# Performance work log

Measured on AMD Instinct MI355X. Metric: run time of the kernel, lower is better.

## Reference

```python
import jax, jax.numpy as jnp
import numpy as np
from math import sqrt

B, N, CS, H, D, K = 8, 256, 512, 8, 64, 32
NB = 2 * K + 1          # no_bins = 65
CT = 2048               # c_transition
INF = 1e9
WL = sqrt(0.5)          # w_L
EPS = 1e-5


def setup_inputs() -> dict:
    key = jax.random.key(0)
    ks = jax.random.split(key, 10)
    sc = 0.02
    return {
        "s": jax.random.normal(ks[0], (B, N, CS), jnp.float32),
        "masks": jnp.ones((B, N), jnp.bool_),
        "wq": jax.random.normal(ks[1], (CS, D * H), jnp.float32) * sc,
        "wk": jax.random.normal(ks[2], (CS, D * H), jnp.float32) * sc,
        "wv": jax.random.normal(ks[3], (CS, D * H), jnp.float32) * sc,
        "wb": jax.random.normal(ks[4], (NB, H), jnp.float32) * sc,
        "wo": jax.random.normal(ks[5], ((NB + D) * H, CS), jnp.float32) * sc,
        "bo": jnp.zeros((CS,), jnp.float32),
        "ln1_g": jnp.ones((CS,), jnp.float32),
        "ln1_b": jnp.zeros((CS,), jnp.float32),
        "w1": jax.random.normal(ks[6], (CS, CT), jnp.float32) * sc,
        "b1": jnp.zeros((CT,), jnp.float32),
        "w2": jax.random.normal(ks[7], (CT, CS), jnp.float32) * sc,
        "b2": jnp.zeros((CS,), jnp.float32),
        "ln2_g": jnp.ones((CS,), jnp.float32),
        "ln2_b": jnp.zeros((CS,), jnp.float32),
    }


def _layernorm(x, g, b):
    m = jnp.mean(x, -1, keepdims=True)
    v = jnp.var(x, -1, keepdims=True)
    return (x - m) * jax.lax.rsqrt(v + EPS) * g + b


def _heads(x):  # [B,N,D*H] -> [B,H,N,D]  (torch: reshape(B,N,D,H) then move H forward)
    return jnp.transpose(x.reshape(B, N, D, H), (0, 3, 1, 2))


def reference(s, masks, wq, wk, wv, wb, wo, bo, ln1_g, ln1_b, w1, b1, w2, b2, ln2_g, ln2_b):
    mf = masks.astype(s.dtype)                       # [B,N]
    sq = mf[:, :, None] * mf[:, None, :]             # [B,N,N]

    # relative position one-hot, clipped to [-K, K] -> [N,N,NB]
    r = jnp.arange(N)
    dmat = jnp.clip(r[:, None] - r[None, :], -K, K) + K
    relpos_base = jax.nn.one_hot(dmat, NB, dtype=s.dtype)
    relpos = relpos_base[None] * sq[..., None]       # [B,N,N,NB]

    b_bias = jnp.einsum('bijc,ch->bhij', relpos, wb)  # [B,H,N,N]

    q = _heads(s @ wq)                               # [B,H,N,D]
    k = _heads(s @ wk)
    v = _heads(s @ wv)

    logits = WL * (jnp.einsum('bhid,bhjd->bhij', q, k) / sqrt(D) + b_bias)
    logits = logits - INF * (1.0 - sq)[:, None]      # mask
    a = jax.nn.softmax(logits, axis=-1)              # [B,H,N,N]

    # pairwise aggregation and value aggregation (einsum avoids [B,H,N,N,NB] blowup)
    o_pair = jnp.einsum('bhij,bijc->bhic', a, relpos)  # [B,H,N,NB]
    o = jnp.einsum('bhij,bhjd->bhid', a, v)            # [B,H,N,D]

    op = jnp.transpose(o_pair, (0, 2, 1, 3)).reshape(B, N, H * NB)
    ov = jnp.transpose(o, (0, 2, 1, 3)).reshape(B, N, H * D)
    embd = jnp.concatenate([op, ov], axis=-1) @ wo + bo   # [B,N,CS]

    x = _layernorm(s + embd, ln1_g, ln1_b)
    ff = jax.nn.relu(x @ w1 + b1) @ w2 + b2
    x = _layernorm(x + ff, ln2_g, ln2_b)
    return x, a
```

## Files before the change

kernel.cpp:

```cpp
#include <hip/hip_runtime.h>
#include <hip/hip_bf16.h>
#include <cstdint>

#define B_ 8
#define N_ 256
#define CS_ 512
#define H_ 8
#define D_ 64
#define K_ 32
#define NB_ 65
#define CT_ 2048
#define WL_ 0.70710678118654752f

typedef __attribute__((ext_vector_type(8))) short bf16x8;
typedef __attribute__((ext_vector_type(4))) float f32x4;

#define GLOBAL_AS __attribute__((address_space(1)))
#define LDS_AS __attribute__((address_space(3)))

__device__ __forceinline__ void async16(void* lds, const void* g) {
  __builtin_amdgcn_global_load_lds((const GLOBAL_AS uint32_t*)g,
                                   (LDS_AS uint32_t*)lds, 16, 0, 0);
}

__device__ __forceinline__ ushort f2bf(float v) {
  __hip_bfloat16 hb = __float2bfloat16(v);
  return *(ushort*)&hb;
}

__device__ __forceinline__ float bf2f(ushort u) {
  union { uint32_t ui; float f; } cv; cv.ui = (uint32_t)u << 16;
  return cv.f;
}

template<int TN>
__device__ __forceinline__ void stage_tile(
    const ushort* __restrict__ A, const ushort* __restrict__ Bt,
    ushort* As, ushort* Bs, int bm, int bn, int Kd, int k0, int srow, int sg) {
  const int RP = TN / 8;
#pragma unroll
  for (int r = 0; r < 64 / RP; ++r) {
    int row = r * RP + srow;
    int gl = sg ^ (row & 7);
    async16(&As[row * 64 + sg * 8], A + (size_t)(bm + row) * Kd + k0 + gl * 8);
  }
#pragma unroll
  for (int r = 0; r < 8; ++r) {
    int row = r * RP + srow;
    int gl = sg ^ (row & 7);
    async16(&Bs[row * 64 + sg * 8], Bt + (size_t)(bn + row) * Kd + k0 + gl * 8);
  }
}

template<int TN>
__global__ __launch_bounds__(TN, 2) void gemm_bf16(
    const ushort* __restrict__ A, const ushort* __restrict__ Bt,
    const float* __restrict__ bias, float* __restrict__ C,
    ushort* __restrict__ Cb, int M, int Nc, int Kd, int flags) {
  __shared__ ushort As[2][64 * 64];
  __shared__ ushort Bs[2][TN * 64];
  int tid = threadIdx.x;
  int bm = blockIdx.y * 64, bn = blockIdx.x * TN;
  int S = gridDim.z, z = blockIdx.z;
  int T = Kd >> 6;
  int it0 = (z * T) / S, it1 = ((z + 1) * T) / S;
  if (flags & 8)  C  += (size_t)z * M * Nc;
  if (flags & 32) Cb += (size_t)z * M * Nc;
  int w = tid >> 6, l = tid & 63;
  int lm = l & 15, lq = l >> 4;
  int srow = tid >> 3;
  int sg = tid & 7;

  f32x4 acc[4][4];
#pragma unroll
  for (int i = 0; i < 4; ++i)
#pragma unroll
    for (int j = 0; j < 4; ++j) acc[i][j] = (f32x4){0.f, 0.f, 0.f, 0.f};

  stage_tile<TN>(A, Bt, &As[0][0], &Bs[0][0], bm, bn, Kd, it0 << 6, srow, sg);

  for (int it = it0; it < it1; ++it) {
    int cur = (it - it0) & 1;
    __syncthreads();
    if (it + 1 < it1) {
      int nxt = cur ^ 1;
      stage_tile<TN>(A, Bt, &As[nxt][0], &Bs[nxt][0], bm, bn, Kd,
                     (it + 1) << 6, srow, sg);
    }
#pragma unroll
    for (int kk = 0; kk < 2; ++kk) {
      bf16x8 af[4], bfr[4];
#pragma unroll
      for (int i = 0; i < 4; ++i) {
        int ma = 16 * i + lm;
        af[i] = *(const bf16x8*)&As[cur][ma * 64 + ((kk * 4 + lq) ^ (ma & 7)) * 8];
        int nb = w * 64 + 16 * i + lm;
        bfr[i] = *(const bf16x8*)&Bs[cur][nb * 64 + ((kk * 4 + lq) ^ (nb & 7)) * 8];
      }
#pragma unroll
      for (int i = 0; i < 4; ++i)
#pragma unroll
        for (int j = 0; j < 4; ++j)
          acc[i][j] = __builtin_amdgcn_mfma_f32_16x16x32_bf16(
              af[i], bfr[j], acc[i][j], 0, 0, 0);
    }
  }
  __syncthreads();

  int bcol0 = bn + w * 64;
  int lr = l >> 3, lc = l & 7;
  ushort* Tb = &Bs[0][w * 4096];

  if (flags & 16) {
    int which = bcol0 >> 9;
    int hh = (bcol0 & 511) >> 6;
    int b = bm >> 8, nn0 = bm & 255;
    if (which == 2) {
#pragma unroll
      for (int j = 0; j < 4; ++j)
#pragma unroll
        for (int i = 0; i < 4; ++i) {
          ushort pk[4];
#pragma unroll
          for (int r = 0; r < 4; ++r) pk[r] = f2bf(acc[i][j][r]);
          *(uint2*)&Tb[(16 * j + lm) * 64 + 16 * i + lq * 4] = *(uint2*)pk;
        }
    } else {
#pragma unroll
      for (int j = 0; j < 4; ++j)
#pragma unroll
        for (int i = 0; i < 4; ++i)
#pragma unroll
          for (int r = 0; r < 4; ++r)
            Tb[(16 * i + lq * 4 + r) * 64 + 16 * j + lm] = f2bf(acc[i][j][r]);
    }
    __asm__ __volatile__("" ::: "memory");
    ushort* dstb = Cb + (size_t)which * 1048576 + (size_t)(b * 8 + hh) * 16384;
#pragma unroll
    for (int p = 0; p < 8; ++p) {
      int rowL = p * 8 + lr;
      bf16x8 vv = *(const bf16x8*)&Tb[rowL * 64 + lc * 8];
      if (which == 2)
        *(bf16x8*)(dstb + (size_t)rowL * 256 + nn0 + lc * 8) = vv;
      else
        *(bf16x8*)(dstb + (size_t)(nn0 + rowL) * 64 + lc * 8) = vv;
    }
    return;
  }
  if (flags & 4) {
#pragma unroll
    for (int j = 0; j < 4; ++j) {
      float bv = ((flags & 1) && z == 0) ? bias[bcol0 + 16 * j + lm] : 0.f;
#pragma unroll
      for (int i = 0; i < 4; ++i)
#pragma unroll
        for (int r = 0; r < 4; ++r) {
          float v = acc[i][j][r] + bv;
          if (flags & 2) v = fmaxf(v, 0.f);
          Tb[(16 * i + lq * 4 + r) * 64 + 16 * j + lm] = f2bf(v);
        }
    }
    __asm__ __volatile__("" ::: "memory");
#pragma unroll
    for (int p = 0; p < 8; ++p) {
      int rowL = p * 8 + lr;
      bf16x8 vv = *(const bf16x8*)&Tb[rowL * 64 + lc * 8];
      *(bf16x8*)(Cb + (size_t)(bm + rowL) * Nc + bcol0 + lc * 8) = vv;
    }
    return;
  }
#pragma unroll
  for (int j = 0; j < 4; ++j) {
    int col = bcol0 + 16 * j + lm;
    float bv = ((flags & 1) && z == 0) ? bias[col] : 0.f;
#pragma unroll
    for (int i = 0; i < 4; ++i)
#pragma unroll
      for (int r = 0; r < 4; ++r) {
        int row = bm + 16 * i + lq * 4 + r;
        float v = acc[i][j][r] + bv;
        if (flags & 2) v = fmaxf(v, 0.f);
        C[(size_t)row * Nc + col] = v;
      }
  }
}

__global__ __launch_bounds__(256) void prep_all(
    const float* __restrict__ s, __hip_bfloat16* __restrict__ s_bf,
    const float* __restrict__ wq, const float* __restrict__ wk,
    const float* __restrict__ wv, const float* __restrict__ wo,
    const float* __restrict__ w1, const float* __restrict__ w2,
    __hip_bfloat16* __restrict__ wqkvT, __hip_bfloat16* __restrict__ wopT,
    __hip_bfloat16* __restrict__ w1T, __hip_bfloat16* __restrict__ w2T) {
  int blk = blockIdx.x;
  if (blk < 512) {
    int i = blk * 256 + threadIdx.x;
    float4 a = ((const float4*)s)[i * 2];
    float4 c = ((const float4*)s)[i * 2 + 1];
    ushort pk[8] = {f2bf(a.x), f2bf(a.y), f2bf(a.z), f2bf(a.w),
                    f2bf(c.x), f2bf(c.y), f2bf(c.z), f2bf(c.w)};
    *(uint4*)&((ushort*)s_bf)[i * 8] = *(uint4*)pk;
    return;
  }
  blk -= 512;
  __shared__ float tile[32][33];
  const float* src;
  __hip_bfloat16* dst;
  int R, C, Kpad, tX, tIdx, whichBase = -1;
  if (blk < 768) {
    int zz = blk >> 8; tIdx = blk & 255;
    src = zz == 0 ? wq : zz == 1 ? wk : wv;
    dst = wqkvT; whichBase = zz * 512; R = 512; C = 512; Kpad = 512; tX = 16;
  } else if (blk < 1312) {
    tIdx = blk - 768; src = wo; dst = wopT; R = 1032; C = 512; Kpad = 1088; tX = 16;
  } else if (blk < 2336) {
    tIdx = blk - 1312; src = w1; dst = w1T; R = 512; C = 2048; Kpad = 512; tX = 64;
  } else {
    tIdx = blk - 2336; src = w2; dst = w2T; R = 2048; C = 512; Kpad = 2048; tX = 16;
  }
  int c0 = (tIdx % tX) * 32, r0 = (tIdx / tX) * 32;
  int tx = threadIdx.x & 7, ty = threadIdx.x >> 3;
  {
    int r = r0 + ty, c = c0 + tx * 4;
    float4 v = (r < R) ? *(const float4*)&src[(size_t)r * C + c]
                       : (float4){0.f, 0.f, 0.f, 0.f};
    tile[ty][tx * 4 + 0] = v.x;
    tile[ty][tx * 4 + 1] = v.y;
    tile[ty][tx * 4 + 2] = v.z;
    tile[ty][tx * 4 + 3] = v.w;
  }
  __syncthreads();
  {
    int cc = c0 + ty;
    int k = r0 + tx * 4;
    float a0 = tile[tx * 4 + 0][ty];
    float a1 = tile[tx * 4 + 1][ty];
    float a2 = tile[tx * 4 + 2][ty];
    float a3 = tile[tx * 4 + 3][ty];
    int n = (whichBase >= 0) ? (whichBase + (cc & 7) * 64 + (cc >> 3)) : cc;
    ushort pk[4] = {f2bf(a0), f2bf(a1), f2bf(a2), f2bf(a3)};
    *(uint2*)&dst[(size_t)n * Kpad + k] = *(uint2*)pk;
  }
}

__global__ __launch_bounds__(128) void attn_fused(
    const ushort* __restrict__ qh, const ushort* __restrict__ kh,
    const ushort* __restrict__ vT, const int* __restrict__ masks,
    const float* __restrict__ wb, float* __restrict__ a_out,
    ushort* __restrict__ cat) {
  int strip = blockIdx.x & 7, bh = blockIdx.x >> 3;
  int h = bh & 7, b = bh >> 3;
  __shared__ ushort Ks[256 * 64];
  __shared__ ushort Ps[32 * 64];
  __shared__ float wbs[NB_];
  __shared__ float mfj[256];
  int tid = threadIdx.x;
  int srow = tid >> 3, sg = tid & 7;
#pragma unroll
  for (int rr = 0; rr < 16; ++rr) {
    int row = rr * 16 + srow;
    int gl = sg ^ (row & 7);
    async16(&Ks[row * 64 + sg * 8],
            kh + ((size_t)bh * 256 + row) * 64 + gl * 8);
  }
  int w = tid >> 6, l = tid & 63, lm = l & 15, lq = l >> 4;
  bf16x8 qf[2];
  {
    const ushort* qrow =
        qh + ((size_t)bh * 256 + strip * 32 + w * 16 + lm) * 64 + lq * 8;
    qf[0] = *(const bf16x8*)qrow;
    qf[1] = *(const bf16x8*)(qrow + 32);
  }
  if (tid < NB_) wbs[tid] = wb[tid * H_ + h];
  mfj[tid]       = (masks[b * 256 + tid] != 0) ? 1.f : 0.f;
  mfj[tid + 128] = (masks[b * 256 + tid + 128] != 0) ? 1.f : 0.f;
  __syncthreads();

  f32x4 acc[16];
#pragma unroll
  for (int ct = 0; ct < 16; ++ct) {
    int krow = ct * 16 + lm;
    bf16x8 kf0 = *(const bf16x8*)&Ks[krow * 64 + ((lq) ^ (krow & 7)) * 8];
    bf16x8 kf1 = *(const bf16x8*)&Ks[krow * 64 + ((4 + lq) ^ (krow & 7)) * 8];
    f32x4 zf = (f32x4){0.f, 0.f, 0.f, 0.f};
    zf = __builtin_amdgcn_mfma_f32_16x16x32_bf16(qf[0], kf0, zf, 0, 0, 0);
    acc[ct] = __builtin_amdgcn_mfma_f32_16x16x32_bf16(qf[1], kf1, zf, 0, 0, 0);
  }
  int ibase = strip * 32 + w * 16 + lq * 4;
  float mfi[4];
#pragma unroll
  for (int r = 0; r < 4; ++r) mfi[r] = mfj[ibase + r];
#pragma unroll
  for (int ct = 0; ct < 16; ++ct) {
    int j = ct * 16 + lm;
    float mj = mfj[j];
#pragma unroll
    for (int r = 0; r < 4; ++r) {
      int i = ibase + r;
      int diff = i - j;
      int cb = diff < -K_ ? 0 : (diff > K_ ? 2 * K_ : diff + K_);
      float sq = mfi[r] * mj;
      acc[ct][r] = WL_ * (acc[ct][r] * 0.125f + wbs[cb] * sq) - 1e9f * (1.f - sq);
    }
  }
  float mx[4], sm[4];
#pragma unroll
  for (int r = 0; r < 4; ++r) {
    float m = acc[0][r];
#pragma unroll
    for (int ct = 1; ct < 16; ++ct) m = fmaxf(m, acc[ct][r]);
#pragma unroll
    for (int o = 1; o < 16; o <<= 1) m = fmaxf(m, __shfl_xor(m, o, 64));
    mx[r] = m;
  }
#pragma unroll
  for (int ct = 0; ct < 16; ++ct)
#pragma unroll
    for (int r = 0; r < 4; ++r) acc[ct][r] = __expf(acc[ct][r] - mx[r]);
#pragma unroll
  for (int r = 0; r < 4; ++r) {
    float s = 0.f;
#pragma unroll
    for (int ct = 0; ct < 16; ++ct) s += acc[ct][r];
#pragma unroll
    for (int o = 1; o < 16; o <<= 1) s += __shfl_xor(s, o, 64);
    sm[r] = 1.f / s;
  }
  float p0[4] = {0.f, 0.f, 0.f, 0.f}, p64[4] = {0.f, 0.f, 0.f, 0.f};
#pragma unroll
  for (int ct = 0; ct < 16; ++ct) {
    int j = ct * 16 + lm;
    float mj = mfj[j];
#pragma unroll
    for (int r = 0; r < 4; ++r) {
      int i = ibase + r;
      float aval = acc[ct][r] * sm[r];
      a_out[((size_t)bh * 256 + i) * 256 + j] = aval;
      float val = aval * mfi[r] * mj;
      int diff = i - j;
      if (diff <= -K_)      p0[r] += val;
      else if (diff >= K_)  p64[r] += val;
      else cat[((size_t)(b * 256 + i)) * 1088 + h * 65 + diff + K_] = f2bf(val);
    }
  }
#pragma unroll
  for (int r = 0; r < 4; ++r)
#pragma unroll
    for (int o = 1; o < 16; o <<= 1) {
      p0[r]  += __shfl_xor(p0[r], o, 64);
      p64[r] += __shfl_xor(p64[r], o, 64);
    }
  if (lm == 0) {
#pragma unroll
    for (int r = 0; r < 4; ++r) {
      int i = ibase + r;
      cat[((size_t)(b * 256 + i)) * 1088 + h * 65 + 0]      = f2bf(p0[r]);
      cat[((size_t)(b * 256 + i)) * 1088 + h * 65 + 2 * K_] = f2bf(p64[r]);
    }
  }
#pragma unroll
  for (int r = 0; r < 4; ++r) {
    int i = ibase + r;
#pragma unroll
    for (int t = 0; t < 4; ++t) {
      int c = 1 + lm + 16 * t;
      if (c < 64) {
        int j = i - c + K_;
        if (j < 0 || j > 255)
          cat[((size_t)(b * 256 + i)) * 1088 + h * 65 + c] = 0;
      }
    }
  }
  if (h == 0) {
    for (int idx = tid; idx < 32 * 56; idx += 128) {
      int r = idx / 56, c = 1032 + (idx - r * 56);
      cat[((size_t)(b * 256 + strip * 32 + r)) * 1088 + c] = 0;
    }
  }
  f32x4 acc2[4];
#pragma unroll
  for (int nt = 0; nt < 4; ++nt) acc2[nt] = (f32x4){0.f, 0.f, 0.f, 0.f};
  const ushort* vbase = vT + (size_t)bh * 16384;
#pragma unroll
  for (int qt = 0; qt < 4; ++qt) {
    bf16x8 vf0[4], vf1[4];
#pragma unroll
    for (int nt = 0; nt < 4; ++nt) {
      const ushort* vrow = vbase + (size_t)(nt * 16 + lm) * 256 + qt * 64 + lq * 8;
      vf0[nt] = *(const bf16x8*)vrow;
      vf1[nt] = *(const bf16x8*)(vrow + 32);
    }
#pragma unroll
    for (int ctl = 0; ctl < 4; ++ctl) {
      int ct = qt * 4 + ctl;
#pragma unroll
      for (int r = 0; r < 4; ++r) {
        int rowl = w * 16 + lq * 4 + r;
        int g = ctl * 2 + (lm >> 3);
        Ps[rowl * 64 + ((g ^ (rowl & 7)) << 3) + (lm & 7)] =
            f2bf(acc[ct][r] * sm[r]);
      }
    }
    int prow = w * 16 + lm;
#pragma unroll
    for (int kst = 0; kst < 2; ++kst) {
      bf16x8 af = *(const bf16x8*)&Ps[prow * 64 + (((kst * 4 + lq) ^ (prow & 7)) << 3)];
#pragma unroll
      for (int nt = 0; nt < 4; ++nt)
        acc2[nt] = __builtin_amdgcn_mfma_f32_16x16x32_bf16(
            af, kst ? vf1[nt] : vf0[nt], acc2[nt], 0, 0, 0);
    }
  }
#pragma unroll
  for (int nt = 0; nt < 4; ++nt) {
    int d = nt * 16 + lm;
#pragma unroll
    for (int r = 0; r < 4; ++r) {
      int i = ibase + r;
      cat[((size_t)(b * 256 + i)) * 1088 + 520 + h * 64 + d] = f2bf(acc2[nt][r]);
    }
  }
}

__global__ __launch_bounds__(128) void ln_sum(
    const float* __restrict__ x1, const ushort* __restrict__ xp,
    int S, int stride, const float* __restrict__ g,
    const float* __restrict__ bta, float* __restrict__ out,
    __hip_bfloat16* __restrict__ out_bf) {
  __shared__ float redA[2], redB[2];
  int row = blockIdx.x, tid = threadIdx.x;
  size_t base = (size_t)row * 512;
  float4 v = *(const float4*)(x1 + base + tid * 4);
  for (int s = 0; s < S; ++s) {
    uint2 p = *(const uint2*)(xp + (size_t)s * stride + base + tid * 4);
    v.x += bf2f((ushort)(p.x & 0xffff));
    v.y += bf2f((ushort)(p.x >> 16));
    v.z += bf2f((ushort)(p.y & 0xffff));
    v.w += bf2f((ushort)(p.y >> 16));
  }
  float su = v.x + v.y + v.z + v.w;
  float sq = v.x * v.x + v.y * v.y + v.z * v.z + v.w * v.w;
#pragma unroll
  for (int o = 32; o > 0; o >>= 1) {
    su += __shfl_xor(su, o, 64);
    sq += __shfl_xor(sq, o, 64);
  }
  int w = tid >> 6;
  if ((tid & 63) == 0) { redA[w] = su; redB[w] = sq; }
  __syncthreads();
  su = redA[0] + redA[1]; sq = redB[0] + redB[1];
  float mean = su * (1.f / 512.f);
  float var = sq * (1.f / 512.f) - mean * mean;
  float inv = rsqrtf(var + 1e-5f);
  float4 gv = *(const float4*)(g + tid * 4);
  float4 bv = *(const float4*)(bta + tid * 4);
  float4 o4;
  o4.x = (v.x - mean) * inv * gv.x + bv.x;
  o4.y = (v.y - mean) * inv * gv.y + bv.y;
  o4.z = (v.z - mean) * inv * gv.z + bv.z;
  o4.w = (v.w - mean) * inv * gv.w + bv.w;
  *(float4*)(out + base + tid * 4) = o4;
  if (out_bf) {
    ushort pk[4] = {f2bf(o4.x), f2bf(o4.y), f2bf(o4.z), f2bf(o4.w)};
    *(uint2*)&((ushort*)out_bf)[base + tid * 4] = *(uint2*)pk;
  }
}

extern "C" void kernel_launch(void* const* d_in, const int* in_sizes, int n_in,
                              void* d_out, int out_size, void* d_ws, size_t ws_size,
                              hipStream_t stream) {
  const float* s     = (const float*)d_in[0];
  const int*   masks = (const int*)d_in[1];
  const float* wq = (const float*)d_in[2];
  const float* wk = (const float*)d_in[3];
  const float* wv = (const float*)d_in[4];
  const float* wb = (const float*)d_in[5];
  const float* wo = (const float*)d_in[6];
  const float* bo = (const float*)d_in[7];
  const float* ln1_g = (const float*)d_in[8];
  const float* ln1_b = (const float*)d_in[9];
  const float* w1 = (const float*)d_in[10];
  const float* b1 = (const float*)d_in[11];
  const float* w2 = (const float*)d_in[12];
  const float* b2 = (const float*)d_in[13];
  const float* ln2_g = (const float*)d_in[14];
  const float* ln2_b = (const float*)d_in[15];

  float* out_x = (float*)d_out;
  float* out_a = out_x + 1048576;

  float* ws = (float*)d_ws;
  ushort* embd_part = (ushort*)(ws + 0);
  float* xbuf       = ws + 4194304;
  ushort* ff_part   = (ushort*)(ws + 5242880);
  ushort* qkv_bf    = (ushort*)(ws + 9437184);
  ushort* q_bf = qkv_bf;
  ushort* k_bf = qkv_bf + 1048576;
  ushort* v_bf = qkv_bf + 2097152;
  ushort* cat_bf = (ushort*)(ws + 10223616);
  __hip_bfloat16* h_bf  = (__hip_bfloat16*)(ws + 11337728);
  __hip_bfloat16* s_bf  = (__hip_bfloat16*)(ws + 13434880);
  __hip_bfloat16* x_bf  = (__hip_bfloat16*)(ws + 13959168);
  __hip_bfloat16* wqkvT = (__hip_bfloat16*)(ws + 14483456);
  __hip_bfloat16* wopT  = (__hip_bfloat16*)(ws + 14876672);
  __hip_bfloat16* w1T   = (__hip_bfloat16*)(ws + 15155200);
  __hip_bfloat16* w2T   = (__hip_bfloat16*)(ws + 15679488);

  dim3 blk(256);
  prep_all<<<dim3(3872), blk, 0, stream>>>(s, s_bf, wq, wk, wv, wo, w1, w2,
                                           wqkvT, wopT, w1T, w2T);
  gemm_bf16<128><<<dim3(12, 32, 1), dim3(128), 0, stream>>>(
      (const ushort*)s_bf, (const ushort*)wqkvT, nullptr, nullptr,
      qkv_bf, 2048, 1536, 512, 16);
  attn_fused<<<dim3(512), dim3(128), 0, stream>>>(q_bf, k_bf, v_bf, masks, wb,
                                                  out_a, cat_bf);
  gemm_bf16<256><<<dim3(2, 32, 8), blk, 0, stream>>>(
      cat_bf, (const ushort*)wopT, bo, nullptr, embd_part,
      2048, 512, 1088, 1 | 4 | 32);
  ln_sum<<<dim3(2048), dim3(128), 0, stream>>>(s, embd_part, 8, 1048576,
                                               ln1_g, ln1_b, xbuf, x_bf);
  gemm_bf16<256><<<dim3(8, 32, 1), blk, 0, stream>>>(
      (const ushort*)x_bf, (const ushort*)w1T, b1, nullptr, (ushort*)h_bf,
      2048, 2048, 512, 1 | 2 | 4);
  gemm_bf16<256><<<dim3(2, 32, 8), blk, 0, stream>>>(
      (const ushort*)h_bf, (const ushort*)w2T, b2, nullptr, ff_part,
      2048, 512, 2048, 1 | 4 | 32);
  ln_sum<<<dim3(2048), dim3(128), 0, stream>>>(xbuf, ff_part, 8, 1048576,
                                               ln2_g, ln2_b, out_x, nullptr);
}
```

Measured before the change: 177.1 us.

## Triple-buffer GEMM LDS pipeline with prefetch depth two, unify tile to 64x128

Replaces the double-buffered GEMM K-loop with a three-stage LDS ring that prefetches two tiles ahead, using an explicit vmcnt wait and a raw barrier instead of __syncthreads. The GEMM template is collapsed to a single 128-thread, 64x128 tile shape. The output and FFN2 split-K GEMMs go from split 8 to split 4, with correspondingly more N blocks, and the layernorm reduction sums 4 partials instead of 8. This aims to hide global-load latency better and cut partial-sum traffic, at the cost of more LDS per block and redundant clamped prefetches at the end of the loop.

```diff
diff --git a/kernel.cpp b/kernel.cpp
--- a/kernel.cpp
+++ b/kernel.cpp
@@ -33,34 +33,31 @@
   return cv.f;
 }
 
-template<int TN>
 __device__ __forceinline__ void stage_tile(
     const ushort* __restrict__ A, const ushort* __restrict__ Bt,
     ushort* As, ushort* Bs, int bm, int bn, int Kd, int k0, int srow, int sg) {
-  const int RP = TN / 8;
-#pragma unroll
-  for (int r = 0; r < 64 / RP; ++r) {
-    int row = r * RP + srow;
+#pragma unroll
+  for (int r = 0; r < 4; ++r) {
+    int row = r * 16 + srow;
     int gl = sg ^ (row & 7);
     async16(&As[row * 64 + sg * 8], A + (size_t)(bm + row) * Kd + k0 + gl * 8);
   }
 #pragma unroll
   for (int r = 0; r < 8; ++r) {
-    int row = r * RP + srow;
+    int row = r * 16 + srow;
     int gl = sg ^ (row & 7);
     async16(&Bs[row * 64 + sg * 8], Bt + (size_t)(bn + row) * Kd + k0 + gl * 8);
   }
 }
 
-template<int TN>
-__global__ __launch_bounds__(TN, 2) void gemm_bf16(
+__global__ __launch_bounds__(128) void gemm_bf16(
     const ushort* __restrict__ A, const ushort* __restrict__ Bt,
     const float* __restrict__ bias, float* __restrict__ C,
     ushort* __restrict__ Cb, int M, int Nc, int Kd, int flags) {
-  __shared__ ushort As[2][64 * 64];
-  __shared__ ushort Bs[2][TN * 64];
+  __shared__ ushort As[3][64 * 64];
+  __shared__ ushort Bs[3][128 * 64];
   int tid = threadIdx.x;
-  int bm = blockIdx.y * 64, bn = blockIdx.x * TN;
+  int bm = blockIdx.y * 64, bn = blockIdx.x * 128;
   int S = gridDim.z, z = blockIdx.z;
   int T = Kd >> 6;
   int it0 = (z * T) / S, it1 = ((z + 1) * T) / S;
@@ -77,25 +74,31 @@
 #pragma unroll
     for (int j = 0; j < 4; ++j) acc[i][j] = (f32x4){0.f, 0.f, 0.f, 0.f};
 
-  stage_tile<TN>(A, Bt, &As[0][0], &Bs[0][0], bm, bn, Kd, it0 << 6, srow, sg);
+  stage_tile(A, Bt, &As[it0 % 3][0], &Bs[it0 % 3][0], bm, bn, Kd,
+             it0 << 6, srow, sg);
+  stage_tile(A, Bt, &As[(it0 + 1) % 3][0], &Bs[(it0 + 1) % 3][0], bm, bn, Kd,
+             (it0 + 1) << 6, srow, sg);
 
   for (int it = it0; it < it1; ++it) {
-    int cur = (it - it0) & 1;
-    __syncthreads();
-    if (it + 1 < it1) {
-      int nxt = cur ^ 1;
-      stage_tile<TN>(A, Bt, &As[nxt][0], &Bs[nxt][0], bm, bn, Kd,
-                     (it + 1) << 6, srow, sg);
-    }
+    asm volatile("s_waitcnt vmcnt(12)" ::: "memory");
+    __builtin_amdgcn_s_barrier();
+    __builtin_amdgcn_sched_barrier(0);
+    {
+      int pf = it + 2;
+      int kt = pf < it1 ? pf : it1 - 1;
+      stage_tile(A, Bt, &As[pf % 3][0], &Bs[pf % 3][0], bm, bn, Kd,
+                 kt << 6, srow, sg);
+    }
+    int cs = it % 3;
 #pragma unroll
     for (int kk = 0; kk < 2; ++kk) {
       bf16x8 af[4], bfr[4];
 #pragma unroll
       for (int i = 0; i < 4; ++i) {
         int ma = 16 * i + lm;
-        af[i] = *(const bf16x8*)&As[cur][ma * 64 + ((kk * 4 + lq) ^ (ma & 7)) * 8];
+        af[i] = *(const bf16x8*)&As[cs][ma * 64 + ((kk * 4 + lq) ^ (ma & 7)) * 8];
         int nb = w * 64 + 16 * i + lm;
-        bfr[i] = *(const bf16x8*)&Bs[cur][nb * 64 + ((kk * 4 + lq) ^ (nb & 7)) * 8];
+        bfr[i] = *(const bf16x8*)&Bs[cs][nb * 64 + ((kk * 4 + lq) ^ (nb & 7)) * 8];
       }
 #pragma unroll
       for (int i = 0; i < 4; ++i)
@@ -506,25 +509,25 @@
   __hip_bfloat16* w1T   = (__hip_bfloat16*)(ws + 15155200);
   __hip_bfloat16* w2T   = (__hip_bfloat16*)(ws + 15679488);
 
-  dim3 blk(256);
+  dim3 blk(256), blkg(128);
   prep_all<<<dim3(3872), blk, 0, stream>>>(s, s_bf, wq, wk, wv, wo, w1, w2,
                                            wqkvT, wopT, w1T, w2T);
-  gemm_bf16<128><<<dim3(12, 32, 1), dim3(128), 0, stream>>>(
+  gemm_bf16<<<dim3(12, 32, 1), blkg, 0, stream>>>(
       (const ushort*)s_bf, (const ushort*)wqkvT, nullptr, nullptr,
       qkv_bf, 2048, 1536, 512, 16);
-  attn_fused<<<dim3(512), dim3(128), 0, stream>>>(q_bf, k_bf, v_bf, masks, wb,
-                                                  out_a, cat_bf);
-  gemm_bf16<256><<<dim3(2, 32, 8), blk, 0, stream>>>(
+  attn_fused<<<dim3(512), blkg, 0, stream>>>(q_bf, k_bf, v_bf, masks, wb,
+                                             out_a, cat_bf);
+  gemm_bf16<<<dim3(4, 32, 4), blkg, 0, stream>>>(
       cat_bf, (const ushort*)wopT, bo, nullptr, embd_part,
       2048, 512, 1088, 1 | 4 | 32);
-  ln_sum<<<dim3(2048), dim3(128), 0, stream>>>(s, embd_part, 8, 1048576,
-                                               ln1_g, ln1_b, xbuf, x_bf);
-  gemm_bf16<256><<<dim3(8, 32, 1), blk, 0, stream>>>(
+  ln_sum<<<dim3(2048), blkg, 0, stream>>>(s, embd_part, 4, 1048576,
+                                          ln1_g, ln1_b, xbuf, x_bf);
+  gemm_bf16<<<dim3(16, 32, 1), blkg, 0, stream>>>(
       (const ushort*)x_bf, (const ushort*)w1T, b1, nullptr, (ushort*)h_bf,
       2048, 2048, 512, 1 | 2 | 4);
-  gemm_bf16<256><<<dim3(2, 32, 8), blk, 0, stream>>>(
+  gemm_bf16<<<dim3(4, 32, 4), blkg, 0, stream>>>(
       (const ushort*)h_bf, (const ushort*)w2T, b2, nullptr, ff_part,
       2048, 512, 2048, 1 | 4 | 32);
-  ln_sum<<<dim3(2048), dim3(128), 0, stream>>>(xbuf, ff_part, 8, 1048576,
-                                               ln2_g, ln2_b, out_x, nullptr);
-}
+  ln_sum<<<dim3(2048), blkg, 0, stream>>>(xbuf, ff_part, 4, 1048576,
+                                          ln2_g, ln2_b, out_x, nullptr);
+}
```

Result: slower. 184.4 us (+4.2%).
